# Optimization experiments

Hardware: AMD Instinct MI355X
Metric: run time of the kernel (lower is better)

Reference implementation:

```python
import jax, jax.numpy as jnp
import numpy as np

DX = 1000.0
DY = 1000.0
EPS = 1e-8


def _weno5(qm2, qm1, q0, qp1, qp2):
    """Classic WENO5 left-biased reconstruction at the face i+1/2."""
    # candidate stencil reconstructions
    f1 = (1.0 / 3.0) * qm2 - (7.0 / 6.0) * qm1 + (11.0 / 6.0) * q0
    f2 = -(1.0 / 6.0) * qm1 + (5.0 / 6.0) * q0 + (1.0 / 3.0) * qp1
    f3 = (1.0 / 3.0) * q0 + (5.0 / 6.0) * qp1 - (1.0 / 6.0) * qp2
    # smoothness indicators
    k1, k2 = 13.0 / 12.0, 0.25
    b1 = k1 * (qm2 - 2.0 * qm1 + q0) ** 2 + k2 * (qm2 - 4.0 * qm1 + 3.0 * q0) ** 2
    b2 = k1 * (qm1 - 2.0 * q0 + qp1) ** 2 + k2 * (qm1 - qp1) ** 2
    b3 = k1 * (q0 - 2.0 * qp1 + qp2) ** 2 + k2 * (3.0 * q0 - 4.0 * qp1 + qp2) ** 2
    # nonlinear weights (ideal weights 1/10, 6/10, 3/10)
    w1 = 0.1 / (b1 + EPS) ** 2
    w2 = 0.6 / (b2 + EPS) ** 2
    w3 = 0.3 / (b3 + EPS) ** 2
    return (w1 * f1 + w2 * f2 + w3 * f3) / (w1 + w2 + w3)


def _flux_along(q, vel, axis):
    """Upwind WENO5 flux vel * q_face at faces i+1/2, one face per cell.

    fe[..., i] = flux at face between cells i and i+1 along `axis`.
    Boundary stencils use edge-replicated ghost cells.
    """
    n = q.shape[axis]
    pad = [(0, 0), (0, 0)]
    pad[axis] = (2, 3)  # left recon needs i-2..i+2, right recon needs i-1..i+3
    qp = jnp.pad(q, pad, mode='edge')

    def s(k):  # q at cell i+k, shape == q.shape
        return jax.lax.slice_in_dim(qp, 2 + k, 2 + k + n, axis=axis)

    q_left = _weno5(s(-2), s(-1), s(0), s(1), s(2))   # upwind for vel >= 0
    q_right = _weno5(s(3), s(2), s(1), s(0), s(-1))   # upwind for vel <  0 (mirrored)
    return vel * jnp.where(vel >= 0.0, q_left, q_right)


def setup_inputs() -> dict:
    key = jax.random.key(0)
    k1, k2, k3 = jax.random.split(key, 3)
    Ny, Nx = 2048, 4096
    h = jax.random.normal(k1, (Ny, Nx), dtype=jnp.float32)
    u = jax.random.normal(k2, (Ny, Nx), dtype=jnp.float32)
    v = jax.random.normal(k3, (Ny, Nx), dtype=jnp.float32)
    return {"h": h, "u": u, "v": v}


def reference(h, u, v):
    # WENO5 upwind fluxes at east (U-point) and north (V-point) faces
    fe = _flux_along(h, u, axis=1)
    fn = _flux_along(h, v, axis=0)
    # tendency -div(h u_vec) on the ghost=2 interior, zero on the ghost ring
    div = (fe[2:-2, 2:-2] - fe[2:-2, 1:-3]) / DX + (fn[2:-2, 2:-2] - fn[1:-3, 2:-2]) / DY
    out = jnp.zeros_like(h).at[2:-2, 2:-2].set(-div)
    return out
```

## Files before the change

kernel.cpp:

```cpp
#include <hip/hip_runtime.h>

#define NX 4096
#define NY 2048
#define EPS 1e-8f
#define ROWS 8
#define CPW 63
#define INV_D 0.001f

__device__ __forceinline__ int clampi(int i, int lo, int hi) {
    return i < lo ? lo : (i > hi ? hi : i);
}

__device__ __forceinline__ float weno5(float qm2, float qm1, float q0, float qp1, float qp2) {
    const float f1 = fmaf(1.0f/3.0f, qm2, fmaf(-7.0f/6.0f, qm1, (11.0f/6.0f)*q0));
    const float f2 = fmaf(-1.0f/6.0f, qm1, fmaf(5.0f/6.0f, q0, (1.0f/3.0f)*qp1));
    const float f3 = fmaf(1.0f/3.0f, q0, fmaf(5.0f/6.0f, qp1, (-1.0f/6.0f)*qp2));
    const float k1 = 13.0f/12.0f, k2 = 0.25f;
    float d1 = qm2 - 2.0f*qm1 + q0;
    float e1 = qm2 - 4.0f*qm1 + 3.0f*q0;
    float d2 = qm1 - 2.0f*q0 + qp1;
    float e2 = qm1 - qp1;
    float d3 = q0 - 2.0f*qp1 + qp2;
    float e3 = 3.0f*q0 - 4.0f*qp1 + qp2;
    float b1 = fmaf(k1, d1*d1, k2*(e1*e1));
    float b2 = fmaf(k1, d2*d2, k2*(e2*e2));
    float b3 = fmaf(k1, d3*d3, k2*(e3*e3));
    float t1 = b1 + EPS, t2 = b2 + EPS, t3 = b3 + EPS;
    float p23 = t2*t3, p13 = t1*t3, p12 = t1*t2;
    float w1 = 0.1f*(p23*p23);
    float w2 = 0.6f*(p13*p13);
    float w3 = 0.3f*(p12*p12);
    float num = fmaf(w1, f1, fmaf(w2, f2, w3*f3));
    float den = (w1 + w2) + w3;
    return num * __builtin_amdgcn_rcpf(den);
}

__device__ __forceinline__ float face_flux(float vel, float hm2, float hm1, float h0,
                                           float hp1, float hp2, float hp3) {
    bool pos = (vel >= 0.0f);
    float a = pos ? hm2 : hp3;
    float b = pos ? hm1 : hp2;
    float c = pos ? h0  : hp1;
    float d = pos ? hp1 : h0;
    float e = pos ? hp2 : hm1;
    return vel * weno5(a, b, c, d, e);
}

__global__ __launch_bounds__(256) void adv_kernel(const float* __restrict__ h,
                                                  const float* __restrict__ u,
                                                  const float* __restrict__ v,
                                                  float* __restrict__ out) {
    const int lane = threadIdx.x & 63;
    const int wid  = threadIdx.x >> 6;
    const int x0 = blockIdx.x * CPW;
    const int xf = x0 - 1 + lane;
    const int xo = x0 + lane;
    const int y0 = (blockIdx.y * 4 + wid) * ROWS;

    int xs0 = clampi(xf - 2, 0, NX - 1);
    int xs1 = clampi(xf - 1, 0, NX - 1);
    int xs2 = clampi(xf,     0, NX - 1);
    int xs3 = clampi(xf + 1, 0, NX - 1);
    int xs4 = clampi(xf + 2, 0, NX - 1);
    int xs5 = clampi(xf + 3, 0, NX - 1);
    const int xc = xo < NX ? xo : NX - 1;

    float w[ROWS + 6];
#pragma unroll
    for (int k = 0; k < ROWS + 6; ++k) {
        int yy = clampi(y0 - 3 + k, 0, NY - 1);
        w[k] = h[(size_t)yy * NX + xc];
    }
    float fn[ROWS + 1];
#pragma unroll
    for (int j = 0; j <= ROWS; ++j) {
        int fy = clampi(y0 - 1 + j, 0, NY - 1);
        float vv = v[(size_t)fy * NX + xc];
        fn[j] = face_flux(vv, w[j], w[j+1], w[j+2], w[j+3], w[j+4], w[j+5]);
    }

#pragma unroll
    for (int r = 0; r < ROWS; ++r) {
        int y = y0 + r;
        const float* hr = h + (size_t)y * NX;
        float fe = face_flux(u[(size_t)y * NX + xs2],
                             hr[xs0], hr[xs1], hr[xs2], hr[xs3], hr[xs4], hr[xs5]);
        float fe_right = __shfl_down(fe, 1);
        if (lane < CPW && xo < NX) {
            float val = 0.0f;
            if (xo >= 2 && xo < NX - 2 && y >= 2 && y < NY - 2) {
                val = -((fe_right - fe) + (fn[r + 1] - fn[r])) * INV_D;
            }
            out[(size_t)y * NX + xo] = val;
        }
    }
}

extern "C" void kernel_launch(void* const* d_in, const int* in_sizes, int n_in,
                              void* d_out, int out_size, void* d_ws, size_t ws_size,
                              hipStream_t stream) {
    const float* h = (const float*)d_in[0];
    const float* u = (const float*)d_in[1];
    const float* v = (const float*)d_in[2];
    float* out = (float*)d_out;

    dim3 block(256, 1, 1);
    dim3 grid((NX + CPW - 1) / CPW, NY / (4 * ROWS), 1);
    adv_kernel<<<grid, block, 0, stream>>>(h, u, v, out);
}
```

Measured before the change: 43.36 us.

## Pack east/north WENO into f32x2, stream rows, and specialize interior blocks

New measurement: 52.05 us. 20.1% more time.

```diff
diff --git a/kernel.cpp b/kernel.cpp
--- a/kernel.cpp
+++ b/kernel.cpp
@@ -3,47 +3,127 @@
 #define NX 4096
 #define NY 2048
 #define EPS 1e-8f
-#define ROWS 8
+#define ROWS 16
 #define CPW 63
 #define INV_D 0.001f
+
+typedef float f32x2 __attribute__((ext_vector_type(2)));
 
 __device__ __forceinline__ int clampi(int i, int lo, int hi) {
     return i < lo ? lo : (i > hi ? hi : i);
 }
 
-__device__ __forceinline__ float weno5(float qm2, float qm1, float q0, float qp1, float qp2) {
-    const float f1 = fmaf(1.0f/3.0f, qm2, fmaf(-7.0f/6.0f, qm1, (11.0f/6.0f)*q0));
-    const float f2 = fmaf(-1.0f/6.0f, qm1, fmaf(5.0f/6.0f, q0, (1.0f/3.0f)*qp1));
-    const float f3 = fmaf(1.0f/3.0f, q0, fmaf(5.0f/6.0f, qp1, (-1.0f/6.0f)*qp2));
+__device__ __forceinline__ f32x2 weno5_pk(f32x2 qm2, f32x2 qm1, f32x2 q0,
+                                          f32x2 qp1, f32x2 qp2) {
+    f32x2 f1 = (1.0f/3.0f)*qm2 - (7.0f/6.0f)*qm1 + (11.0f/6.0f)*q0;
+    f32x2 f2 = (-1.0f/6.0f)*qm1 + (5.0f/6.0f)*q0 + (1.0f/3.0f)*qp1;
+    f32x2 f3 = (1.0f/3.0f)*q0 + (5.0f/6.0f)*qp1 - (1.0f/6.0f)*qp2;
+    f32x2 d1 = qm2 - 2.0f*qm1 + q0;
+    f32x2 e1 = qm2 - 4.0f*qm1 + 3.0f*q0;
+    f32x2 d2 = qm1 - 2.0f*q0 + qp1;
+    f32x2 e2 = qm1 - qp1;
+    f32x2 d3 = q0 - 2.0f*qp1 + qp2;
+    f32x2 e3 = 3.0f*q0 - 4.0f*qp1 + qp2;
     const float k1 = 13.0f/12.0f, k2 = 0.25f;
-    float d1 = qm2 - 2.0f*qm1 + q0;
-    float e1 = qm2 - 4.0f*qm1 + 3.0f*q0;
-    float d2 = qm1 - 2.0f*q0 + qp1;
-    float e2 = qm1 - qp1;
-    float d3 = q0 - 2.0f*qp1 + qp2;
-    float e3 = 3.0f*q0 - 4.0f*qp1 + qp2;
-    float b1 = fmaf(k1, d1*d1, k2*(e1*e1));
-    float b2 = fmaf(k1, d2*d2, k2*(e2*e2));
-    float b3 = fmaf(k1, d3*d3, k2*(e3*e3));
-    float t1 = b1 + EPS, t2 = b2 + EPS, t3 = b3 + EPS;
-    float p23 = t2*t3, p13 = t1*t3, p12 = t1*t2;
-    float w1 = 0.1f*(p23*p23);
-    float w2 = 0.6f*(p13*p13);
-    float w3 = 0.3f*(p12*p12);
-    float num = fmaf(w1, f1, fmaf(w2, f2, w3*f3));
-    float den = (w1 + w2) + w3;
-    return num * __builtin_amdgcn_rcpf(den);
+    f32x2 b1 = k1*(d1*d1) + k2*(e1*e1);
+    f32x2 b2 = k1*(d2*d2) + k2*(e2*e2);
+    f32x2 b3 = k1*(d3*d3) + k2*(e3*e3);
+    f32x2 t1 = b1 + EPS, t2 = b2 + EPS, t3 = b3 + EPS;
+    f32x2 p23 = t2*t3, p13 = t1*t3, p12 = t1*t2;
+    f32x2 w1 = 0.1f*(p23*p23);
+    f32x2 w2 = 0.6f*(p13*p13);
+    f32x2 w3 = 0.3f*(p12*p12);
+    f32x2 num = w1*f1 + w2*f2 + w3*f3;
+    f32x2 den = (w1 + w2) + w3;
+    f32x2 rc;
+    rc.x = __builtin_amdgcn_rcpf(den.x);
+    rc.y = __builtin_amdgcn_rcpf(den.y);
+    return num * rc;
 }
 
-__device__ __forceinline__ float face_flux(float vel, float hm2, float hm1, float h0,
-                                           float hp1, float hp2, float hp3) {
-    bool pos = (vel >= 0.0f);
-    float a = pos ? hm2 : hp3;
-    float b = pos ? hm1 : hp2;
-    float c = pos ? h0  : hp1;
-    float d = pos ? hp1 : h0;
-    float e = pos ? hp2 : hm1;
-    return vel * weno5(a, b, c, d, e);
+template <bool EDGE>
+__device__ __forceinline__ void run_strip(const float* __restrict__ h,
+                                          const float* __restrict__ u,
+                                          const float* __restrict__ v,
+                                          float* __restrict__ out,
+                                          int x0, int y0w, int lane) {
+    const int xf = x0 - 1 + lane;
+    const int xo = x0 + lane;
+    const int xc = EDGE ? (xo < NX ? xo : NX - 1) : xo;
+    const int xq = EDGE ? clampi(xf, 0, NX - 1) : xf;
+
+    int xs[6];
+    if (EDGE) {
+#pragma unroll
+        for (int k = 0; k < 6; ++k) xs[k] = clampi(xf - 2 + k, 0, NX - 1);
+    }
+
+    float hw[6];
+#pragma unroll
+    for (int k = 0; k < 6; ++k) {
+        int yy = EDGE ? clampi(y0w - 3 + k, 0, NY - 1) : (y0w - 3 + k);
+        hw[k] = h[(size_t)yy * NX + xc];
+    }
+    float fn_prev;
+    {
+        int fy = EDGE ? clampi(y0w - 1, 0, NY - 1) : (y0w - 1);
+        float vv = v[(size_t)fy * NX + xc];
+        bool vp = (vv >= 0.0f);
+        f32x2 a = { vp ? hw[0] : hw[5], vp ? hw[0] : hw[5] };
+        f32x2 b = { vp ? hw[1] : hw[4], vp ? hw[1] : hw[4] };
+        f32x2 c = { vp ? hw[2] : hw[3], vp ? hw[2] : hw[3] };
+        f32x2 d = { vp ? hw[3] : hw[2], vp ? hw[3] : hw[2] };
+        f32x2 e = { vp ? hw[4] : hw[1], vp ? hw[4] : hw[1] };
+        fn_prev = vv * weno5_pk(a, b, c, d, e).x;
+    }
+
+#pragma unroll
+    for (int r = 0; r < ROWS; ++r) {
+        const int y = y0w + r;
+        const size_t rowb = (size_t)y * NX;
+
+        float r0, r1, r2, r3, r4, r5;
+        if (EDGE) {
+            const float* hr = h + rowb;
+            r0 = hr[xs[0]]; r1 = hr[xs[1]]; r2 = hr[xs[2]];
+            r3 = hr[xs[3]]; r4 = hr[xs[4]]; r5 = hr[xs[5]];
+        } else {
+            const float* hr = h + rowb + xf;
+            r0 = hr[-2]; r1 = hr[-1]; r2 = hr[0];
+            r3 = hr[1];  r4 = hr[2];  r5 = hr[3];
+        }
+        float uval = __builtin_nontemporal_load(u + rowb + xq);
+        float vval = __builtin_nontemporal_load(v + rowb + xc);
+        int yy = EDGE ? clampi(y + 3, 0, NY - 1) : (y + 3);
+        float hwn = h[(size_t)yy * NX + xc];
+
+        bool up = (uval >= 0.0f);
+        bool vp = (vval >= 0.0f);
+        f32x2 a = { up ? r0 : r5, vp ? hw[1] : hwn   };
+        f32x2 b = { up ? r1 : r4, vp ? hw[2] : hw[5] };
+        f32x2 c = { up ? r2 : r3, vp ? hw[3] : hw[4] };
+        f32x2 d = { up ? r3 : r2, vp ? hw[4] : hw[3] };
+        f32x2 e = { up ? r4 : r1, vp ? hw[5] : hw[2] };
+        f32x2 q = weno5_pk(a, b, c, d, e);
+        float fe = uval * q.x;
+        float fn_cur = vval * q.y;
+
+        float fe_r = __shfl_down(fe, 1);
+        float val = ((fe - fe_r) + (fn_prev - fn_cur)) * INV_D;
+
+        if (EDGE) {
+            if (xo < 2 || xo >= NX - 2 || y < 2 || y >= NY - 2) val = 0.0f;
+            if (lane < CPW && xo < NX)
+                __builtin_nontemporal_store(val, out + rowb + xo);
+        } else {
+            if (lane < CPW)
+                __builtin_nontemporal_store(val, out + rowb + xo);
+        }
+
+        hw[0] = hw[1]; hw[1] = hw[2]; hw[2] = hw[3];
+        hw[3] = hw[4]; hw[4] = hw[5]; hw[5] = hwn;
+        fn_prev = fn_cur;
+    }
 }
 
 __global__ __launch_bounds__(256) void adv_kernel(const float* __restrict__ h,
@@ -53,47 +133,14 @@
     const int lane = threadIdx.x & 63;
     const int wid  = threadIdx.x >> 6;
     const int x0 = blockIdx.x * CPW;
-    const int xf = x0 - 1 + lane;
-    const int xo = x0 + lane;
-    const int y0 = (blockIdx.y * 4 + wid) * ROWS;
+    const int y0w = (blockIdx.y * 4 + wid) * ROWS;
 
-    int xs0 = clampi(xf - 2, 0, NX - 1);
-    int xs1 = clampi(xf - 1, 0, NX - 1);
-    int xs2 = clampi(xf,     0, NX - 1);
-    int xs3 = clampi(xf + 1, 0, NX - 1);
-    int xs4 = clampi(xf + 2, 0, NX - 1);
-    int xs5 = clampi(xf + 3, 0, NX - 1);
-    const int xc = xo < NX ? xo : NX - 1;
-
-    float w[ROWS + 6];
-#pragma unroll
-    for (int k = 0; k < ROWS + 6; ++k) {
-        int yy = clampi(y0 - 3 + k, 0, NY - 1);
-        w[k] = h[(size_t)yy * NX + xc];
-    }
-    float fn[ROWS + 1];
-#pragma unroll
-    for (int j = 0; j <= ROWS; ++j) {
-        int fy = clampi(y0 - 1 + j, 0, NY - 1);
-        float vv = v[(size_t)fy * NX + xc];
-        fn[j] = face_flux(vv, w[j], w[j+1], w[j+2], w[j+3], w[j+4], w[j+5]);
-    }
-
-#pragma unroll
-    for (int r = 0; r < ROWS; ++r) {
-        int y = y0 + r;
-        const float* hr = h + (size_t)y * NX;
-        float fe = face_flux(u[(size_t)y * NX + xs2],
-                             hr[xs0], hr[xs1], hr[xs2], hr[xs3], hr[xs4], hr[xs5]);
-        float fe_right = __shfl_down(fe, 1);
-        if (lane < CPW && xo < NX) {
-            float val = 0.0f;
-            if (xo >= 2 && xo < NX - 2 && y >= 2 && y < NY - 2) {
-                val = -((fe_right - fe) + (fn[r + 1] - fn[r])) * INV_D;
-            }
-            out[(size_t)y * NX + xo] = val;
-        }
-    }
+    const bool edge = (blockIdx.x == 0) || (blockIdx.x >= 64) ||
+                      (blockIdx.y == 0) || (blockIdx.y == gridDim.y - 1);
+    if (edge)
+        run_strip<true>(h, u, v, out, x0, y0w, lane);
+    else
+        run_strip<false>(h, u, v, out, x0, y0w, lane);
 }
 
 extern "C" void kernel_launch(void* const* d_in, const int* in_sizes, int n_in,
```
